# Optimization experiments

Hardware: AMD Instinct MI355X
Metric: run time of the kernel (lower is better)

Reference implementation:

```python
import jax, jax.numpy as jnp
import numpy as np

B, S, D = 16, 2048, 128

def setup_inputs() -> dict:
    key = jax.random.key(0)
    kq, kk, kv = jax.random.split(key, 3)
    queries = jax.random.normal(kq, (B, S, D), dtype=jnp.float32)
    keys = jax.random.normal(kk, (B, S, D), dtype=jnp.float32)
    values = jax.random.normal(kv, (B, S, D), dtype=jnp.float32)
    return {"queries": queries, "keys": keys, "values": values}

def reference(queries, keys, values):
    # scores: [B, S, S] = Q @ K^T / sqrt(D)
    d = queries.shape[-1]
    scores = jnp.einsum('bqd,bkd->bqk', queries, keys) / jnp.float32(np.sqrt(d))
    attn = jax.nn.softmax(scores, axis=-1)
    # dropout_rate=0.0 -> identity
    out = jnp.einsum('bqk,bkd->bqd', attn, values)
    return out
```

## Files before the change

### kernel.cpp

```cpp
#include <hip/hip_runtime.h>
#include <hip/hip_bf16.h>

#define BATCH 16
#define SEQ   2048
#define DIM   128
#define KTILE 64
#define QT    128
#define SCALE 0.08838834764831845f

typedef __bf16 bf16_t;
typedef __bf16 bf16x8 __attribute__((ext_vector_type(8)));
typedef float  f32x4  __attribute__((ext_vector_type(4)));

#define KSTR 136
#define VSTR 72

__device__ __forceinline__ int rho(int s) {
    return (s & 32) | ((s & 4) << 2) | (((s >> 3) & 3) << 2) | (s & 3);
}

__global__ __launch_bounds__(256, 1)
void attn_fwd(const float* __restrict__ Qg, const float* __restrict__ Kg,
              const float* __restrict__ Vg, float* __restrict__ Og)
{
    __shared__ __align__(16) bf16_t sK [KTILE][KSTR];
    __shared__ __align__(16) bf16_t sVt[DIM][VSTR];

    const int tid  = threadIdx.x;
    const int wave = tid >> 6;
    const int lane = tid & 63;
    const int l16  = lane & 15;
    const int g    = lane >> 4;

    const int bid   = blockIdx.x;
    const int batch = ((bid & 7) << 1) | ((bid >> 7) & 1);
    const int qtile = (bid >> 3) & 15;

    const float* Kb = Kg + (size_t)batch * SEQ * DIM;
    const float* Vb = Vg + (size_t)batch * SEQ * DIM;

    bf16x8 qf[2][4];
    #pragma unroll
    for (int grp = 0; grp < 2; ++grp) {
        const float* qp = Qg + ((size_t)batch * SEQ + qtile * QT + wave * 32
                                + grp * 16 + l16) * DIM + g * 8;
        #pragma unroll
        for (int c = 0; c < 4; ++c) {
            const float4 u = *reinterpret_cast<const float4*>(qp + c * 32);
            const float4 v = *reinterpret_cast<const float4*>(qp + c * 32 + 4);
            bf16x8 f;
            f[0] = (bf16_t)(u.x * SCALE); f[1] = (bf16_t)(u.y * SCALE);
            f[2] = (bf16_t)(u.z * SCALE); f[3] = (bf16_t)(u.w * SCALE);
            f[4] = (bf16_t)(v.x * SCALE); f[5] = (bf16_t)(v.y * SCALE);
            f[6] = (bf16_t)(v.z * SCALE); f[7] = (bf16_t)(v.w * SCALE);
            qf[grp][c] = f;
        }
    }

    const int krow0 = tid >> 4;
    const int kch   = tid & 15;
    const int vkg   = tid >> 5;
    const int vd4   = tid & 31;

    float4 ka[4][2];
    float4 va[8];

    auto load_tile = [&](int k0) {
        #pragma unroll
        for (int i = 0; i < 4; ++i) {
            const float* p = Kb + (size_t)(k0 + krow0 + i * 16) * DIM + kch * 8;
            ka[i][0] = *reinterpret_cast<const float4*>(p);
            ka[i][1] = *reinterpret_cast<const float4*>(p + 4);
        }
        #pragma unroll
        for (int j = 0; j < 8; ++j)
            va[j] = *reinterpret_cast<const float4*>(
                Vb + (size_t)(k0 + vkg * 8 + j) * DIM + vd4 * 4);
    };

    load_tile(0);

    const f32x4 vzero = {0.f, 0.f, 0.f, 0.f};
    f32x4 o[2][8];
    #pragma unroll
    for (int grp = 0; grp < 2; ++grp)
        #pragma unroll
        for (int i = 0; i < 8; ++i) o[grp][i] = vzero;
    float lsum[2] = {0.f, 0.f};

    for (int k0 = 0; k0 < SEQ; k0 += KTILE) {
        __syncthreads();

        #pragma unroll
        for (int i = 0; i < 4; ++i) {
            const float* a = reinterpret_cast<const float*>(&ka[i][0]);
            bf16x8 w;
            #pragma unroll
            for (int e = 0; e < 8; ++e) w[e] = (bf16_t)a[e];
            *reinterpret_cast<bf16x8*>(&sK[rho(krow0 + i * 16)][kch * 8]) = w;
        }
        #pragma unroll
        for (int dd = 0; dd < 4; ++dd) {
            bf16x8 w;
            #pragma unroll
            for (int j = 0; j < 8; ++j)
                w[j] = (bf16_t)(reinterpret_cast<const float*>(&va[j])[dd]);
            *reinterpret_cast<bf16x8*>(&sVt[vd4 * 4 + dd][vkg * 8]) = w;
        }
        __syncthreads();

        const int k0n = (k0 + KTILE < SEQ) ? (k0 + KTILE) : 0;
        load_tile(k0n);

        f32x4 sc[2][4];
        #pragma unroll
        for (int grp = 0; grp < 2; ++grp)
            #pragma unroll
            for (int ksb = 0; ksb < 4; ++ksb) sc[grp][ksb] = vzero;
        #pragma unroll
        for (int c = 0; c < 4; ++c) {
            #pragma unroll
            for (int ksb = 0; ksb < 4; ++ksb) {
                bf16x8 kf = *reinterpret_cast<const bf16x8*>(
                    &sK[ksb * 16 + l16][c * 32 + g * 8]);
                sc[0][ksb] = __builtin_amdgcn_mfma_f32_16x16x32_bf16(
                    kf, qf[0][c], sc[0][ksb], 0, 0, 0);
                sc[1][ksb] = __builtin_amdgcn_mfma_f32_16x16x32_bf16(
                    kf, qf[1][c], sc[1][ksb], 0, 0, 0);
            }
        }

        bf16x8 pb[2][2];
        #pragma unroll
        for (int grp = 0; grp < 2; ++grp) {
            float pe[16];
            #pragma unroll
            for (int ksb = 0; ksb < 4; ++ksb) {
                #pragma unroll
                for (int r = 0; r < 4; ++r) {
                    const float p = __expf(sc[grp][ksb][r]);
                    pe[ksb * 4 + r] = p;
                    lsum[grp] += p;
                }
            }
            #pragma unroll
            for (int c2 = 0; c2 < 2; ++c2) {
                bf16x8 t;
                #pragma unroll
                for (int jj = 0; jj < 8; ++jj)
                    t[jj] = (bf16_t)pe[(2 * c2 + (jj >> 2)) * 4 + (jj & 3)];
                pb[grp][c2] = t;
            }
        }

        #pragma unroll
        for (int n0 = 0; n0 < 8; ++n0) {
            #pragma unroll
            for (int c2 = 0; c2 < 2; ++c2) {
                bf16x8 vf = *reinterpret_cast<const bf16x8*>(
                    &sVt[n0 * 16 + l16][c2 * 32 + g * 8]);
                o[0][n0] = __builtin_amdgcn_mfma_f32_16x16x32_bf16(
                    vf, pb[0][c2], o[0][n0], 0, 0, 0);
                o[1][n0] = __builtin_amdgcn_mfma_f32_16x16x32_bf16(
                    vf, pb[1][c2], o[1][n0], 0, 0, 0);
            }
        }
    }

    #pragma unroll
    for (int grp = 0; grp < 2; ++grp) {
        float l = lsum[grp];
        l += __shfl_xor(l, 16);
        l += __shfl_xor(l, 32);
        const float inv = 1.f / l;
        const int q = qtile * QT + wave * 32 + grp * 16 + l16;
        float* op = Og + ((size_t)batch * SEQ + q) * DIM + g * 4;
        #pragma unroll
        for (int n0 = 0; n0 < 8; ++n0) {
            float4 st = { o[grp][n0][0] * inv, o[grp][n0][1] * inv,
                          o[grp][n0][2] * inv, o[grp][n0][3] * inv };
            *reinterpret_cast<float4*>(op + n0 * 16) = st;
        }
    }
}

extern "C" void kernel_launch(void* const* d_in, const int* in_sizes, int n_in,
                              void* d_out, int out_size, void* d_ws, size_t ws_size,
                              hipStream_t stream) {
    const float* Q = (const float*)d_in[0];
    const float* K = (const float*)d_in[1];
    const float* V = (const float*)d_in[2];
    float* O = (float*)d_out;
    dim3 grid(BATCH * SEQ / QT);
    dim3 block(256);
    hipLaunchKernelGGL(attn_fwd, grid, block, 0, stream, Q, K, V, O);
}
```

Before: 153.6 us.

## Split KV sequence across two wave groups with double-buffered LDS and final reduction

Doubles the block to 512 threads: two groups of four waves each process alternating 64-key tiles for the same 128 queries. K/V tiles are double-buffered in shared memory per group, and the V layout gets an XOR swizzle to cut bank conflicts. The partial outputs and row sums are then combined through shared memory before normalisation. This is meant to raise waves per CU and hide load and convert latency, at the cost of a large LDS footprint and an extra reduction pass.

```diff
diff --git a/kernel.cpp b/kernel.cpp
--- a/kernel.cpp
+++ b/kernel.cpp
@@ -5,7 +5,7 @@
 #define SEQ   2048
 #define DIM   128
 #define KTILE 64
-#define QT    128
+#define NSUP  16
 #define SCALE 0.08838834764831845f
 
 typedef __bf16 bf16_t;
@@ -13,28 +13,35 @@
 typedef float  f32x4  __attribute__((ext_vector_type(4)));
 
 #define KSTR 136
-#define VSTR 72
 
 __device__ __forceinline__ int rho(int s) {
     return (s & 32) | ((s & 4) << 2) | (((s >> 3) & 3) << 2) | (s & 3);
 }
-
-__global__ __launch_bounds__(256, 1)
+__device__ __forceinline__ int swz2(int row) {
+    return (row & 7) ^ ((row >> 3) & 7);
+}
+
+__global__ __launch_bounds__(512, 2)
 void attn_fwd(const float* __restrict__ Qg, const float* __restrict__ Kg,
               const float* __restrict__ Vg, float* __restrict__ Og)
 {
-    __shared__ __align__(16) bf16_t sK [KTILE][KSTR];
-    __shared__ __align__(16) bf16_t sVt[DIM][VSTR];
+    __shared__ __align__(16) char smem[135168];
+    bf16_t* sKb = (bf16_t*)smem;
+    bf16_t* sVb = (bf16_t*)(smem + 69632);
 
     const int tid  = threadIdx.x;
     const int wave = tid >> 6;
     const int lane = tid & 63;
     const int l16  = lane & 15;
     const int g    = lane >> 4;
+    const int gr   = wave >> 2;
+    const int w4   = wave & 3;
+    const int t8   = tid & 255;
 
     const int bid   = blockIdx.x;
     const int batch = ((bid & 7) << 1) | ((bid >> 7) & 1);
     const int qtile = (bid >> 3) & 15;
+    const int q0    = qtile * 128 + w4 * 32;
 
     const float* Kb = Kg + (size_t)batch * SEQ * DIM;
     const float* Vb = Vg + (size_t)batch * SEQ * DIM;
@@ -42,8 +49,7 @@
     bf16x8 qf[2][4];
     #pragma unroll
     for (int grp = 0; grp < 2; ++grp) {
-        const float* qp = Qg + ((size_t)batch * SEQ + qtile * QT + wave * 32
-                                + grp * 16 + l16) * DIM + g * 8;
+        const float* qp = Qg + ((size_t)batch * SEQ + q0 + grp * 16 + l16) * DIM + g * 8;
         #pragma unroll
         for (int c = 0; c < 4; ++c) {
             const float4 u = *reinterpret_cast<const float4*>(qp + c * 32);
@@ -57,28 +63,55 @@
         }
     }
 
-    const int krow0 = tid >> 4;
-    const int kch   = tid & 15;
-    const int vkg   = tid >> 5;
-    const int vd4   = tid & 31;
-
-    float4 ka[4][2];
+    const int krow2 = t8 >> 3;
+    const int kch   = t8 & 7;
+    const int vkg   = t8 >> 5;
+    const int vd4   = t8 & 31;
+
+    float4 ka[2][2][2];
     float4 va[8];
 
     auto load_tile = [&](int k0) {
         #pragma unroll
-        for (int i = 0; i < 4; ++i) {
-            const float* p = Kb + (size_t)(k0 + krow0 + i * 16) * DIM + kch * 8;
-            ka[i][0] = *reinterpret_cast<const float4*>(p);
-            ka[i][1] = *reinterpret_cast<const float4*>(p + 4);
-        }
+        for (int rh = 0; rh < 2; ++rh)
+            #pragma unroll
+            for (int ch = 0; ch < 2; ++ch) {
+                const float* p = Kb + (size_t)(k0 + krow2 + rh * 32) * DIM
+                               + kch * 8 + ch * 64;
+                ka[rh][ch][0] = *reinterpret_cast<const float4*>(p);
+                ka[rh][ch][1] = *reinterpret_cast<const float4*>(p + 4);
+            }
         #pragma unroll
         for (int j = 0; j < 8; ++j)
             va[j] = *reinterpret_cast<const float4*>(
                 Vb + (size_t)(k0 + vkg * 8 + j) * DIM + vd4 * 4);
     };
-
-    load_tile(0);
+    auto write_tile = [&](int buf) {
+        #pragma unroll
+        for (int rh = 0; rh < 2; ++rh) {
+            const int row = rho(krow2 + rh * 32);
+            #pragma unroll
+            for (int ch = 0; ch < 2; ++ch) {
+                const float* a = reinterpret_cast<const float*>(&ka[rh][ch][0]);
+                bf16x8 w;
+                #pragma unroll
+                for (int e = 0; e < 8; ++e) w[e] = (bf16_t)a[e];
+                *reinterpret_cast<bf16x8*>(
+                    sKb + (((gr * 2 + buf) * 64 + row) * KSTR) + kch * 8 + ch * 64) = w;
+            }
+        }
+        #pragma unroll
+        for (int dd = 0; dd < 4; ++dd) {
+            const int row = vd4 * 4 + dd;
+            bf16x8 w;
+            #pragma unroll
+            for (int j = 0; j < 8; ++j)
+                w[j] = (bf16_t)(reinterpret_cast<const float*>(&va[j])[dd]);
+            *reinterpret_cast<bf16x8*>(
+                sVb + (((gr * 2 + buf) * 128 + row) * 64)
+                    + ((vkg ^ swz2(row)) << 3)) = w;
+        }
+    };
 
     const f32x4 vzero = {0.f, 0.f, 0.f, 0.f};
     f32x4 o[2][8];
@@ -88,29 +121,18 @@
         for (int i = 0; i < 8; ++i) o[grp][i] = vzero;
     float lsum[2] = {0.f, 0.f};
 
-    for (int k0 = 0; k0 < SEQ; k0 += KTILE) {
+    load_tile(gr * KTILE);
+    write_tile(0);
+    load_tile(128 + gr * KTILE);
+
+    for (int it = 0; it < NSUP; ++it) {
         __syncthreads();
-
-        #pragma unroll
-        for (int i = 0; i < 4; ++i) {
-            const float* a = reinterpret_cast<const float*>(&ka[i][0]);
-            bf16x8 w;
-            #pragma unroll
-            for (int e = 0; e < 8; ++e) w[e] = (bf16_t)a[e];
-            *reinterpret_cast<bf16x8*>(&sK[rho(krow0 + i * 16)][kch * 8]) = w;
-        }
-        #pragma unroll
-        for (int dd = 0; dd < 4; ++dd) {
-            bf16x8 w;
-            #pragma unroll
-            for (int j = 0; j < 8; ++j)
-                w[j] = (bf16_t)(reinterpret_cast<const float*>(&va[j])[dd]);
-            *reinterpret_cast<bf16x8*>(&sVt[vd4 * 4 + dd][vkg * 8]) = w;
-        }
-        __syncthreads();
-
-        const int k0n = (k0 + KTILE < SEQ) ? (k0 + KTILE) : 0;
-        load_tile(k0n);
+        if (it + 1 < NSUP) {
+            write_tile((it + 1) & 1);
+            if (it + 2 < NSUP) load_tile((it + 2) * 128 + gr * KTILE);
+        }
+        const int kbase = (gr * 2 + (it & 1)) * 64;
+        const int vbase = (gr * 2 + (it & 1)) * 128;
 
         f32x4 sc[2][4];
         #pragma unroll
@@ -122,7 +144,7 @@
             #pragma unroll
             for (int ksb = 0; ksb < 4; ++ksb) {
                 bf16x8 kf = *reinterpret_cast<const bf16x8*>(
-                    &sK[ksb * 16 + l16][c * 32 + g * 8]);
+                    sKb + ((kbase + ksb * 16 + l16) * KSTR) + c * 32 + g * 8);
                 sc[0][ksb] = __builtin_amdgcn_mfma_f32_16x16x32_bf16(
                     kf, qf[0][c], sc[0][ksb], 0, 0, 0);
                 sc[1][ksb] = __builtin_amdgcn_mfma_f32_16x16x32_bf16(
@@ -135,14 +157,13 @@
         for (int grp = 0; grp < 2; ++grp) {
             float pe[16];
             #pragma unroll
-            for (int ksb = 0; ksb < 4; ++ksb) {
+            for (int ksb = 0; ksb < 4; ++ksb)
                 #pragma unroll
                 for (int r = 0; r < 4; ++r) {
                     const float p = __expf(sc[grp][ksb][r]);
                     pe[ksb * 4 + r] = p;
                     lsum[grp] += p;
                 }
-            }
             #pragma unroll
             for (int c2 = 0; c2 < 2; ++c2) {
                 bf16x8 t;
@@ -155,10 +176,11 @@
 
         #pragma unroll
         for (int n0 = 0; n0 < 8; ++n0) {
+            const int row = n0 * 16 + l16;
             #pragma unroll
             for (int c2 = 0; c2 < 2; ++c2) {
                 bf16x8 vf = *reinterpret_cast<const bf16x8*>(
-                    &sVt[n0 * 16 + l16][c2 * 32 + g * 8]);
+                    sVb + ((vbase + row) * 64) + (((c2 * 4 + g) ^ swz2(row)) << 3));
                 o[0][n0] = __builtin_amdgcn_mfma_f32_16x16x32_bf16(
                     vf, pb[0][c2], o[0][n0], 0, 0, 0);
                 o[1][n0] = __builtin_amdgcn_mfma_f32_16x16x32_bf16(
@@ -167,19 +189,44 @@
         }
     }
 
-    #pragma unroll
-    for (int grp = 0; grp < 2; ++grp) {
-        float l = lsum[grp];
-        l += __shfl_xor(l, 16);
-        l += __shfl_xor(l, 32);
-        const float inv = 1.f / l;
-        const int q = qtile * QT + wave * 32 + grp * 16 + l16;
-        float* op = Og + ((size_t)batch * SEQ + q) * DIM + g * 4;
-        #pragma unroll
-        for (int n0 = 0; n0 < 8; ++n0) {
-            float4 st = { o[grp][n0][0] * inv, o[grp][n0][1] * inv,
-                          o[grp][n0][2] * inv, o[grp][n0][3] * inv };
-            *reinterpret_cast<float4*>(op + n0 * 16) = st;
+    __syncthreads();
+    float* sf = (float*)smem;
+    float* wb = sf + w4 * 4224;
+    if (gr == 1) {
+        #pragma unroll
+        for (int grp = 0; grp < 2; ++grp)
+            #pragma unroll
+            for (int n0 = 0; n0 < 8; ++n0)
+                *reinterpret_cast<f32x4*>(wb + (grp * 8 + n0) * 256 + lane * 4)
+                    = o[grp][n0];
+        wb[4096 + lane * 2]     = lsum[0];
+        wb[4096 + lane * 2 + 1] = lsum[1];
+    }
+    __syncthreads();
+    if (gr == 0) {
+        #pragma unroll
+        for (int grp = 0; grp < 2; ++grp)
+            #pragma unroll
+            for (int n0 = 0; n0 < 8; ++n0) {
+                f32x4 t = *reinterpret_cast<const f32x4*>(
+                    wb + (grp * 8 + n0) * 256 + lane * 4);
+                o[grp][n0] += t;
+            }
+        lsum[0] += wb[4096 + lane * 2];
+        lsum[1] += wb[4096 + lane * 2 + 1];
+        #pragma unroll
+        for (int grp = 0; grp < 2; ++grp) {
+            float l = lsum[grp];
+            l += __shfl_xor(l, 16);
+            l += __shfl_xor(l, 32);
+            const float inv = 1.f / l;
+            float* op = Og + ((size_t)batch * SEQ + q0 + grp * 16 + l16) * DIM + g * 4;
+            #pragma unroll
+            for (int n0 = 0; n0 < 8; ++n0) {
+                float4 st = { o[grp][n0][0] * inv, o[grp][n0][1] * inv,
+                              o[grp][n0][2] * inv, o[grp][n0][3] * inv };
+                *reinterpret_cast<float4*>(op + n0 * 16) = st;
+            }
         }
     }
 }
@@ -191,7 +238,7 @@
     const float* K = (const float*)d_in[1];
     const float* V = (const float*)d_in[2];
     float* O = (float*)d_out;
-    dim3 grid(BATCH * SEQ / QT);
-    dim3 block(256);
+    dim3 grid(BATCH * SEQ / 128);
+    dim3 block(512);
     hipLaunchKernelGGL(attn_fwd, grid, block, 0, stream, Q, K, V, O);
 }
```

New measurement: 140.4 us. -8.6%, faster.

## Split KV range across two blocks with workspace merge and double-buffered LDS

Applied to the files above, without the earlier changes.

Splits each query tile's key range in half across two blocks, giving 512 blocks instead of 256 so the grid better fills the GPU. Partial outputs and row sums go to a workspace, and an atomic counter lets the second finisher combine them. Since there is no running max, merging is a plain sum. It also double-buffers the K/V tiles in LDS to remove one barrier per iteration and XOR-swizzles the V-transpose layout to reduce bank conflicts. The cost is extra workspace traffic, a memset launch and a small merge epilogue, and the new path only runs when the workspace is large enough.

```diff
diff --git a/kernel.cpp b/kernel.cpp
--- a/kernel.cpp
+++ b/kernel.cpp
@@ -5,7 +5,6 @@
 #define SEQ   2048
 #define DIM   128
 #define KTILE 64
-#define QT    128
 #define SCALE 0.08838834764831845f
 
 typedef __bf16 bf16_t;
@@ -13,18 +12,30 @@
 typedef float  f32x4  __attribute__((ext_vector_type(4)));
 
 #define KSTR 136
-#define VSTR 72
+
+#define NTILE   256
+#define TILE_F  16384
+#define WSO_F   (2 * NTILE * TILE_F)
+#define WSL_F   (2 * NTILE * 128)
+#define WS_NEED ((size_t)(WSO_F + WSL_F + NTILE) * 4)
 
 __device__ __forceinline__ int rho(int s) {
     return (s & 32) | ((s & 4) << 2) | (((s >> 3) & 3) << 2) | (s & 3);
 }
-
-__global__ __launch_bounds__(256, 1)
+__device__ __forceinline__ int swz2(int row) {
+    return (row & 7) ^ ((row >> 3) & 7);
+}
+
+template <int SPLIT>
+__global__ __launch_bounds__(256, 2)
 void attn_fwd(const float* __restrict__ Qg, const float* __restrict__ Kg,
-              const float* __restrict__ Vg, float* __restrict__ Og)
+              const float* __restrict__ Vg, float* __restrict__ Og,
+              float* __restrict__ wsO, float* __restrict__ wsL,
+              int* __restrict__ cnt)
 {
-    __shared__ __align__(16) bf16_t sK [KTILE][KSTR];
-    __shared__ __align__(16) bf16_t sVt[DIM][VSTR];
+    __shared__ __align__(16) bf16_t sK [2][KTILE][KSTR];
+    __shared__ __align__(16) bf16_t sVt[2][DIM][64];
+    __shared__ int sFlag;
 
     const int tid  = threadIdx.x;
     const int wave = tid >> 6;
@@ -33,8 +44,13 @@
     const int g    = lane >> 4;
 
     const int bid   = blockIdx.x;
-    const int batch = ((bid & 7) << 1) | ((bid >> 7) & 1);
-    const int qtile = (bid >> 3) & 15;
+    const int batch = SPLIT ? (((bid & 7) << 1) | ((bid >> 8) & 1))
+                            : (((bid & 7) << 1) | ((bid >> 7) & 1));
+    const int gr    = SPLIT ? ((bid >> 3) & 1) : 0;
+    const int qtile = SPLIT ? ((bid >> 4) & 15) : ((bid >> 3) & 15);
+    const int q0    = qtile * 128 + wave * 32;
+    const int kbeg  = gr * (SEQ / 2);
+    const int nit   = SPLIT ? (SEQ / 2 / KTILE) : (SEQ / KTILE);
 
     const float* Kb = Kg + (size_t)batch * SEQ * DIM;
     const float* Vb = Vg + (size_t)batch * SEQ * DIM;
@@ -42,8 +58,7 @@
     bf16x8 qf[2][4];
     #pragma unroll
     for (int grp = 0; grp < 2; ++grp) {
-        const float* qp = Qg + ((size_t)batch * SEQ + qtile * QT + wave * 32
-                                + grp * 16 + l16) * DIM + g * 8;
+        const float* qp = Qg + ((size_t)batch * SEQ + q0 + grp * 16 + l16) * DIM + g * 8;
         #pragma unroll
         for (int c = 0; c < 4; ++c) {
             const float4 u = *reinterpret_cast<const float4*>(qp + c * 32);
@@ -57,28 +72,50 @@
         }
     }
 
-    const int krow0 = tid >> 4;
-    const int kch   = tid & 15;
-    const int vkg   = tid >> 5;
-    const int vd4   = tid & 31;
-
-    float4 ka[4][2];
-    float4 va[8];
+    const int krow = tid >> 2;
+    const int kq   = tid & 3;
+    const int vkg  = tid >> 5;
+    const int vd4  = tid & 31;
+
+    bf16x8 kst[4];
+    bf16x8 vst[4];
 
     auto load_tile = [&](int k0) {
         #pragma unroll
         for (int i = 0; i < 4; ++i) {
-            const float* p = Kb + (size_t)(k0 + krow0 + i * 16) * DIM + kch * 8;
-            ka[i][0] = *reinterpret_cast<const float4*>(p);
-            ka[i][1] = *reinterpret_cast<const float4*>(p + 4);
-        }
+            const float* p = Kb + (size_t)(k0 + krow) * DIM + kq * 32 + i * 8;
+            const float4 u = *reinterpret_cast<const float4*>(p);
+            const float4 v = *reinterpret_cast<const float4*>(p + 4);
+            bf16x8 f;
+            f[0] = (bf16_t)u.x; f[1] = (bf16_t)u.y; f[2] = (bf16_t)u.z; f[3] = (bf16_t)u.w;
+            f[4] = (bf16_t)v.x; f[5] = (bf16_t)v.y; f[6] = (bf16_t)v.z; f[7] = (bf16_t)v.w;
+            kst[i] = f;
+        }
+        float4 t[8];
         #pragma unroll
         for (int j = 0; j < 8; ++j)
-            va[j] = *reinterpret_cast<const float4*>(
+            t[j] = *reinterpret_cast<const float4*>(
                 Vb + (size_t)(k0 + vkg * 8 + j) * DIM + vd4 * 4);
+        #pragma unroll
+        for (int dd = 0; dd < 4; ++dd) {
+            bf16x8 f;
+            #pragma unroll
+            for (int j = 0; j < 8; ++j)
+                f[j] = (bf16_t)(reinterpret_cast<const float*>(&t[j])[dd]);
+            vst[dd] = f;
+        }
     };
-
-    load_tile(0);
+    auto write_tile = [&](int buf) {
+        const int krr = rho(krow);
+        #pragma unroll
+        for (int i = 0; i < 4; ++i)
+            *reinterpret_cast<bf16x8*>(&sK[buf][krr][kq * 32 + i * 8]) = kst[i];
+        #pragma unroll
+        for (int dd = 0; dd < 4; ++dd) {
+            const int row = vd4 * 4 + dd;
+            *reinterpret_cast<bf16x8*>(&sVt[buf][row][(vkg ^ swz2(row)) << 3]) = vst[dd];
+        }
+    };
 
     const f32x4 vzero = {0.f, 0.f, 0.f, 0.f};
     f32x4 o[2][8];
@@ -88,29 +125,17 @@
         for (int i = 0; i < 8; ++i) o[grp][i] = vzero;
     float lsum[2] = {0.f, 0.f};
 
-    for (int k0 = 0; k0 < SEQ; k0 += KTILE) {
+    load_tile(kbeg);
+    write_tile(0);
+    load_tile(kbeg + KTILE);
+
+    for (int it = 0; it < nit; ++it) {
         __syncthreads();
-
-        #pragma unroll
-        for (int i = 0; i < 4; ++i) {
-            const float* a = reinterpret_cast<const float*>(&ka[i][0]);
-            bf16x8 w;
-            #pragma unroll
-            for (int e = 0; e < 8; ++e) w[e] = (bf16_t)a[e];
-            *reinterpret_cast<bf16x8*>(&sK[rho(krow0 + i * 16)][kch * 8]) = w;
-        }
-        #pragma unroll
-        for (int dd = 0; dd < 4; ++dd) {
-            bf16x8 w;
-            #pragma unroll
-            for (int j = 0; j < 8; ++j)
-                w[j] = (bf16_t)(reinterpret_cast<const float*>(&va[j])[dd]);
-            *reinterpret_cast<bf16x8*>(&sVt[vd4 * 4 + dd][vkg * 8]) = w;
-        }
-        __syncthreads();
-
-        const int k0n = (k0 + KTILE < SEQ) ? (k0 + KTILE) : 0;
-        load_tile(k0n);
+        if (it + 1 < nit) {
+            write_tile((it + 1) & 1);
+            if (it + 2 < nit) load_tile(kbeg + (it + 2) * KTILE);
+        }
+        const int cur = it & 1;
 
         f32x4 sc[2][4];
         #pragma unroll
@@ -122,7 +147,7 @@
             #pragma unroll
             for (int ksb = 0; ksb < 4; ++ksb) {
                 bf16x8 kf = *reinterpret_cast<const bf16x8*>(
-                    &sK[ksb * 16 + l16][c * 32 + g * 8]);
+                    &sK[cur][ksb * 16 + l16][c * 32 + g * 8]);
                 sc[0][ksb] = __builtin_amdgcn_mfma_f32_16x16x32_bf16(
                     kf, qf[0][c], sc[0][ksb], 0, 0, 0);
                 sc[1][ksb] = __builtin_amdgcn_mfma_f32_16x16x32_bf16(
@@ -135,14 +160,13 @@
         for (int grp = 0; grp < 2; ++grp) {
             float pe[16];
             #pragma unroll
-            for (int ksb = 0; ksb < 4; ++ksb) {
+            for (int ksb = 0; ksb < 4; ++ksb)
                 #pragma unroll
                 for (int r = 0; r < 4; ++r) {
                     const float p = __expf(sc[grp][ksb][r]);
                     pe[ksb * 4 + r] = p;
                     lsum[grp] += p;
                 }
-            }
             #pragma unroll
             for (int c2 = 0; c2 < 2; ++c2) {
                 bf16x8 t;
@@ -155,10 +179,11 @@
 
         #pragma unroll
         for (int n0 = 0; n0 < 8; ++n0) {
+            const int row = n0 * 16 + l16;
             #pragma unroll
             for (int c2 = 0; c2 < 2; ++c2) {
                 bf16x8 vf = *reinterpret_cast<const bf16x8*>(
-                    &sVt[n0 * 16 + l16][c2 * 32 + g * 8]);
+                    &sVt[cur][row][((c2 * 4 + g) ^ swz2(row)) << 3]);
                 o[0][n0] = __builtin_amdgcn_mfma_f32_16x16x32_bf16(
                     vf, pb[0][c2], o[0][n0], 0, 0, 0);
                 o[1][n0] = __builtin_amdgcn_mfma_f32_16x16x32_bf16(
@@ -167,19 +192,67 @@
         }
     }
 
+    float lq[2];
     #pragma unroll
     for (int grp = 0; grp < 2; ++grp) {
         float l = lsum[grp];
         l += __shfl_xor(l, 16);
         l += __shfl_xor(l, 32);
-        const float inv = 1.f / l;
-        const int q = qtile * QT + wave * 32 + grp * 16 + l16;
-        float* op = Og + ((size_t)batch * SEQ + q) * DIM + g * 4;
-        #pragma unroll
-        for (int n0 = 0; n0 < 8; ++n0) {
-            float4 st = { o[grp][n0][0] * inv, o[grp][n0][1] * inv,
-                          o[grp][n0][2] * inv, o[grp][n0][3] * inv };
-            *reinterpret_cast<float4*>(op + n0 * 16) = st;
+        lq[grp] = l;
+    }
+
+    if (!SPLIT) {
+        #pragma unroll
+        for (int grp = 0; grp < 2; ++grp) {
+            const float inv = 1.f / lq[grp];
+            float* op = Og + ((size_t)batch * SEQ + q0 + grp * 16 + l16) * DIM + g * 4;
+            #pragma unroll
+            for (int n0 = 0; n0 < 8; ++n0) {
+                float4 st = { o[grp][n0][0] * inv, o[grp][n0][1] * inv,
+                              o[grp][n0][2] * inv, o[grp][n0][3] * inv };
+                *reinterpret_cast<float4*>(op + n0 * 16) = st;
+            }
+        }
+        return;
+    }
+
+    const int tile = batch * 16 + qtile;
+    float* myO = wsO + ((size_t)gr * NTILE + tile) * TILE_F;
+    float* myL = wsL + ((size_t)gr * NTILE + tile) * 128;
+    #pragma unroll
+    for (int grp = 0; grp < 2; ++grp) {
+        #pragma unroll
+        for (int n0 = 0; n0 < 8; ++n0)
+            *reinterpret_cast<f32x4*>(
+                myO + (((wave * 2 + grp) * 8 + n0) << 8) + lane * 4) = o[grp][n0];
+        if (g == 0) myL[wave * 32 + grp * 16 + l16] = lq[grp];
+    }
+    __syncthreads();
+    if (tid == 0) {
+        __threadfence();
+        sFlag = __hip_atomic_fetch_add(&cnt[tile], 1, __ATOMIC_ACQ_REL,
+                                       __HIP_MEMORY_SCOPE_AGENT);
+    }
+    __syncthreads();
+    if (sFlag == 1) {
+        __threadfence();
+        const float* pO = wsO + ((size_t)(1 - gr) * NTILE + tile) * TILE_F;
+        const float* pL = wsL + ((size_t)(1 - gr) * NTILE + tile) * 128;
+        #pragma unroll
+        for (int grp = 0; grp < 2; ++grp) {
+            const float lp  = pL[wave * 32 + grp * 16 + l16];
+            const float inv = 1.f / (lq[grp] + lp);
+            float* op = Og + ((size_t)batch * SEQ + q0 + grp * 16 + l16) * DIM + g * 4;
+            #pragma unroll
+            for (int n0 = 0; n0 < 8; ++n0) {
+                const f32x4 t = *reinterpret_cast<const f32x4*>(
+                    pO + (((wave * 2 + grp) * 8 + n0) << 8) + lane * 4);
+                float4 st = { (o[grp][n0][0] + t[0]) * inv,
+                              (o[grp][n0][1] + t[1]) * inv,
+                              (o[grp][n0][2] + t[2]) * inv,
+                              (o[grp][n0][3] + t[3]) * inv };
+                *reinterpret_cast<float4*>(op + n0 * 16) = st;
+            }
         }
     }
 }
@@ -191,7 +264,16 @@
     const float* K = (const float*)d_in[1];
     const float* V = (const float*)d_in[2];
     float* O = (float*)d_out;
-    dim3 grid(BATCH * SEQ / QT);
-    dim3 block(256);
-    hipLaunchKernelGGL(attn_fwd, grid, block, 0, stream, Q, K, V, O);
-}
+    if (ws_size >= WS_NEED) {
+        float* wsO = (float*)d_ws;
+        float* wsL = wsO + WSO_F;
+        int*   cnt = (int*)(wsL + WSL_F);
+        hipMemsetAsync(cnt, 0, NTILE * sizeof(int), stream);
+        hipLaunchKernelGGL(attn_fwd<1>, dim3(512), dim3(256), 0, stream,
+                           Q, K, V, O, wsO, wsL, cnt);
+    } else {
+        hipLaunchKernelGGL(attn_fwd<0>, dim3(256), dim3(256), 0, stream,
+                           Q, K, V, O, (float*)nullptr, (float*)nullptr,
+                           (int*)nullptr);
+    }
+}
```

Result: slower. 214.0 us (+39.3%).
